# Kernel tuning notes

Measured on AMD Instinct MI355X. Metric: run time of the kernel, lower is better.

## Reference

```python
import jax, jax.numpy as jnp
import numpy as np

D = 1024
H = 16
HD = D // H  # 64


def setup_inputs() -> dict:
    key = jax.random.key(0)
    k1, k2, k3 = jax.random.split(key, 3)
    x = jax.random.normal(k1, (2, 2048, D), dtype=jnp.float32)
    # fused QKV projection weight [d, 3d] and output projection [d, d], no bias
    Wqkv = jax.random.normal(k2, (D, 3 * D), dtype=jnp.float32) * (1.0 / np.sqrt(D))
    Wo = jax.random.normal(k3, (D, D), dtype=jnp.float32) * (1.0 / np.sqrt(D))
    return {"x": x, "Wqkv": Wqkv, "Wo": Wo}


def reference(x, Wqkv, Wo):
    b, t, d = x.shape
    qkv = x @ Wqkv  # [b, t, 3d]
    q, k, v = jnp.split(qkv, 3, axis=-1)
    # [b, t, d] -> [b, h, t, hd]
    def heads(z):
        return z.reshape(b, t, H, HD).transpose(0, 2, 1, 3)
    q, k, v = heads(q), heads(k), heads(v)
    scale = 1.0 / np.sqrt(HD)
    att = jnp.einsum('bhqd,bhkd->bhqk', q, k) * scale  # [b, h, t, t]
    att = jax.nn.softmax(att, axis=-1)
    y = jnp.einsum('bhqk,bhkd->bhqd', att, v)  # [b, h, t, hd]
    y = y.transpose(0, 2, 1, 3).reshape(b, t, d)  # [b, t, d]
    return y @ Wo
```

## Files before the change

### kernel.cpp

```cpp
#include <hip/hip_runtime.h>
#include <hip/hip_bf16.h>

#define D_MODEL 1024
#define NHEADS  16
#define HD      64
#define BATCH   2
#define SEQ     2048
#define NTOK    (BATCH * SEQ)

typedef __attribute__((ext_vector_type(8))) short bf16x8;
typedef __attribute__((ext_vector_type(4))) float f32x4;

#if __has_builtin(__builtin_amdgcn_exp2f)
#define EXP2F(x) __builtin_amdgcn_exp2f(x)
#else
#define EXP2F(x) exp2f(x)
#endif

static __device__ __forceinline__ short f2bf(float f) {
    union { float f; unsigned u; } x; x.f = f;
    unsigned r = (x.u + 0x7fffu + ((x.u >> 16) & 1u)) >> 16;
    return (short)r;
}

static __device__ __forceinline__ unsigned pk_bf16(float a, float b) {
    __hip_bfloat162 h2 = __float22bfloat162_rn(make_float2(a, b));
    union { __hip_bfloat162 h; unsigned u; } c; c.h = h2;
    return c.u;
}

static __device__ __forceinline__ void gl_lds16(const short* g, short* l) {
    __builtin_amdgcn_global_load_lds((const __attribute__((address_space(1))) void*)g,
                                     (__attribute__((address_space(3))) void*)l,
                                     16, 0, 0);
}

__global__ __launch_bounds__(256) void prep_kernel(const float* __restrict__ x,
                                                   short* __restrict__ x_bf,
                                                   const float* __restrict__ Wqkv,
                                                   short* __restrict__ WqkvT,
                                                   const float* __restrict__ Wo,
                                                   short* __restrict__ WoT,
                                                   float cexp) {
    int bid = blockIdx.x;
    int tid = threadIdx.x;

    if (bid < 4096) {
        int i = bid * 256 + tid;
        float4 v = ((const float4*)x)[i];
        short4 o;
        o.x = f2bf(v.x); o.y = f2bf(v.y); o.z = f2bf(v.z); o.w = f2bf(v.w);
        ((short4*)x_bf)[i] = o;
        return;
    }

    __shared__ float tile[32][33];
    const float* in; short* out; int R, C, slimit; float sc; int bx, by;
    if (bid < 4096 + 3072) {
        int idx = bid - 4096;
        in = Wqkv; out = WqkvT; R = D_MODEL; C = 3 * D_MODEL;
        slimit = D_MODEL; sc = cexp;
        bx = idx % 96; by = idx / 96;
    } else {
        int idx = bid - 7168;
        in = Wo; out = WoT; R = D_MODEL; C = D_MODEL;
        slimit = 0; sc = 1.0f;
        bx = idx % 32; by = idx / 32;
    }
    int bc = bx * 32, br = by * 32;
    int tx = tid & 31, ty = tid >> 5;
    #pragma unroll
    for (int i = 0; i < 32; i += 8)
        tile[ty + i][tx] = in[(long)(br + ty + i) * C + bc + tx];
    __syncthreads();
    #pragma unroll
    for (int i = 0; i < 32; i += 8) {
        int orow = bc + ty + i;
        float v = tile[tx][ty + i];
        if (orow < slimit) v *= sc;
        out[(long)orow * R + br + tx] = f2bf(v);
    }
}

__global__ __launch_bounds__(256) void gemm_out(const short* __restrict__ A,
                                                const short* __restrict__ BT,
                                                float* __restrict__ C,
                                                int M, int N, int K) {
    __shared__ short As[128 * 32];
    __shared__ short Bs[64 * 32];

    int tid  = threadIdx.x;
    int lane = tid & 63;
    int w    = tid >> 6;
    int quad = lane >> 4;
    int l16  = lane & 15;

    int m_blk = blockIdx.y * 128, n_blk = blockIdx.x * 64;

    const short* Ag = A  + (long)(m_blk + w * 32 + (lane >> 2)) * K + (lane & 3) * 8;
    const short* Bg = BT + (long)(n_blk + w * 16 + (lane >> 2)) * K + (lane & 3) * 8;
    short* AsW = &As[(w * 32) * 32];
    short* BsW = &Bs[(w * 16) * 32];

    f32x4 acc[2][4] = {};

    for (int k0 = 0; k0 < K; k0 += 32) {
        __syncthreads();
        gl_lds16(Ag + k0,          AsW);
        gl_lds16(Ag + 16 * K + k0, AsW + 16 * 32);
        gl_lds16(Bg + k0,          BsW);
        __syncthreads();

        bf16x8 a[2], b[4];
        #pragma unroll
        for (int i = 0; i < 2; i++)
            a[i] = *(const bf16x8*)&As[(w * 32 + i * 16 + l16) * 32 + quad * 8];
        #pragma unroll
        for (int j = 0; j < 4; j++)
            b[j] = *(const bf16x8*)&Bs[(j * 16 + l16) * 32 + quad * 8];
        #pragma unroll
        for (int i = 0; i < 2; i++)
            #pragma unroll
            for (int j = 0; j < 4; j++)
                acc[i][j] = __builtin_amdgcn_mfma_f32_16x16x32_bf16(a[i], b[j], acc[i][j], 0, 0, 0);
    }

    #pragma unroll
    for (int i = 0; i < 2; i++)
        #pragma unroll
        for (int j = 0; j < 4; j++)
            #pragma unroll
            for (int r = 0; r < 4; r++) {
                int row = m_blk + w * 32 + i * 16 + quad * 4 + r;
                int col = n_blk + j * 16 + l16;
                C[(long)row * N + col] = acc[i][j][r];
            }
}

__global__ __launch_bounds__(256) void gemm_qkv(const short* __restrict__ A,
                                                const short* __restrict__ BT,
                                                short* __restrict__ Qb,
                                                short* __restrict__ Kt2,
                                                short* __restrict__ Vt2) {
    const int K = 1024;
    __shared__ union {
        struct { short As[128 * 32]; short Bs[128 * 32]; } g;
        short Tl[4][64][72];
    } sh;

    int tid  = threadIdx.x;
    int lane = tid & 63;
    int w    = tid >> 6;
    int quad = lane >> 4;
    int l16  = lane & 15;

    int m_blk = blockIdx.y * 128, n_blk = blockIdx.x * 128;
    int mh = (w >> 1) * 64, nh = (w & 1) * 64;

    int sel = blockIdx.x >> 3;
    int ncol0 = n_blk - sel * 1024;

    const short* Ag = A  + (long)(m_blk + w * 32 + (lane >> 2)) * K + (lane & 3) * 8;
    const short* Bg = BT + (long)(n_blk + w * 32 + (lane >> 2)) * K + (lane & 3) * 8;
    short* AsW = &sh.g.As[(w * 32) * 32];
    short* BsW = &sh.g.Bs[(w * 32) * 32];

    f32x4 acc[4][4] = {};

    for (int k0 = 0; k0 < K; k0 += 32) {
        __syncthreads();
        gl_lds16(Ag + k0,          AsW);
        gl_lds16(Ag + 16 * K + k0, AsW + 16 * 32);
        gl_lds16(Bg + k0,          BsW);
        gl_lds16(Bg + 16 * K + k0, BsW + 16 * 32);
        __syncthreads();

        bf16x8 a[4], b[4];
        #pragma unroll
        for (int i = 0; i < 4; i++)
            a[i] = *(const bf16x8*)&sh.g.As[(mh + i * 16 + l16) * 32 + quad * 8];
        #pragma unroll
        for (int j = 0; j < 4; j++)
            b[j] = *(const bf16x8*)&sh.g.Bs[(nh + j * 16 + l16) * 32 + quad * 8];
        #pragma unroll
        for (int i = 0; i < 4; i++)
            #pragma unroll
            for (int j = 0; j < 4; j++)
                acc[i][j] = __builtin_amdgcn_mfma_f32_16x16x32_bf16(a[i], b[j], acc[i][j], 0, 0, 0);
    }

    __syncthreads();

    #pragma unroll
    for (int i = 0; i < 4; i++)
        #pragma unroll
        for (int j = 0; j < 4; j++)
            #pragma unroll
            for (int r = 0; r < 4; r++)
                sh.Tl[w][i * 16 + quad * 4 + r][j * 16 + l16] = f2bf(acc[i][j][r]);

    int R0q = m_blk + mh;
    if (sel == 0) {
        long qbase = (long)R0q * 1024 + (ncol0 + nh);
        #pragma unroll
        for (int ch = 0; ch < 8; ch++) {
            int row  = ch * 8 + (lane >> 3);
            int col0 = (lane & 7) * 8;
            *(bf16x8*)(Qb + qbase + (long)row * 1024 + col0) =
                *(const bf16x8*)&sh.Tl[w][row][col0];
        }
    } else {
        int b2 = R0q >> 11;
        int t  = (R0q & 2047) >> 6;
        int h  = (ncol0 + nh) >> 6;
        long obase = (long)(b2 * 16 + h) * (SEQ * 64) + (long)t * 4096;
        short* outT = (sel == 1) ? Kt2 : Vt2;
        if (sel == 1) {
            #pragma unroll
            for (int ch = 0; ch < 8; ch++) {
                int o = lane * 64 + ch * 8;
                int u = o >> 9, qd = (o >> 7) & 3, l = (o >> 3) & 15;
                int row = (u >> 2) * 32 + ((u >> 1) & 1) * 16 + l;
                int col = (u & 1) * 32 + qd * 8;
                *(bf16x8*)(outT + obase + o) = *(const bf16x8*)&sh.Tl[w][row][col];
            }
        } else {
            #pragma unroll
            for (int ch = 0; ch < 8; ch++) {
                int o = lane * 64 + ch * 8;
                int c = o >> 11, j2 = (o >> 9) & 3, qd = (o >> 7) & 3, l = (o >> 3) & 15;
                int hd = j2 * 16 + l;
                bf16x8 ov;
                #pragma unroll
                for (int jj = 0; jj < 8; jj++) {
                    int s = c * 32 + qd * 8 + jj;
                    int key = (s >> 2) + ((s & 3) << 4);
                    ov[jj] = sh.Tl[w][key][hd];
                }
                *(bf16x8*)(outT + obase + o) = ov;
            }
        }
    }
}

__global__ __launch_bounds__(256, 4) void flash_attn(const short* __restrict__ Qb,
                                                     const short* __restrict__ Kt2,
                                                     const short* __restrict__ Vt2,
                                                     short* __restrict__ y) {
    int tid  = threadIdx.x;
    int lane = tid & 63;
    int w    = tid >> 6;
    int quad = lane >> 4;
    int l16  = lane & 15;
    int qsel = w & 1;
    int ksel = w >> 1;

    int bh = blockIdx.y;
    int b  = bh >> 4;
    int h  = bh & 15;
    int qw = blockIdx.x * 64 + qsel * 32;

    __shared__ union {
        short Ps[4][32 * 72];
        float Mg[2][64][41];
    } sh;
    short* PsW = &sh.Ps[w][0];

    const short* Qrow = Qb + ((long)b * SEQ + qw + l16) * 1024 + h * 64;
    bf16x8 aQ[2][2];
    #pragma unroll
    for (int m = 0; m < 2; m++)
        #pragma unroll
        for (int c = 0; c < 2; c++)
            aQ[m][c] = *(const bf16x8*)(Qrow + (long)(m * 16) * 1024 + c * 32 + quad * 8);

    const short* Ktb = Kt2 + (long)bh * (SEQ * 64) + (long)ksel * 16 * 4096;
    const short* Vtb = Vt2 + (long)bh * (SEQ * 64) + (long)ksel * 16 * 4096;

    f32x4 O[2][4] = {};
    f32x4 Lacc[2] = {};
    bf16x8 ones;
    #pragma unroll
    for (int i = 0; i < 8; i++) ones[i] = (short)0x3F80;

    for (int t = 0; t < 16; t++) {
        const short* Kt = Ktb + t * 4096;
        const short* Vt = Vtb + t * 4096;

        bf16x8 kf[8];
        #pragma unroll
        for (int u = 0; u < 8; u++) kf[u] = *(const bf16x8*)(Kt + u * 512 + lane * 8);

        f32x4 z[2][4];
        #pragma unroll
        for (int m = 0; m < 2; m++)
            #pragma unroll
            for (int kc = 0; kc < 4; kc++) {
                f32x4 zz = {};
                zz = __builtin_amdgcn_mfma_f32_16x16x32_bf16(aQ[m][0], kf[2 * kc],     zz, 0, 0, 0);
                z[m][kc] = __builtin_amdgcn_mfma_f32_16x16x32_bf16(aQ[m][1], kf[2 * kc + 1], zz, 0, 0, 0);
            }

        bf16x8 vf[8];
        #pragma unroll
        for (int u = 0; u < 8; u++) vf[u] = *(const bf16x8*)(Vt + u * 512 + lane * 8);

        #pragma unroll
        for (int m = 0; m < 2; m++)
            #pragma unroll
            for (int r = 0; r < 4; r++) {
                unsigned d0 = pk_bf16(EXP2F(z[m][0][r]), EXP2F(z[m][1][r]));
                unsigned d1 = pk_bf16(EXP2F(z[m][2][r]), EXP2F(z[m][3][r]));
                unsigned long long dd = ((unsigned long long)d1 << 32) | d0;
                *(unsigned long long*)((unsigned*)PsW + (m * 16 + quad * 4 + r) * 36 + 2 * l16) = dd;
            }

        #pragma unroll
        for (int c = 0; c < 2; c++) {
            bf16x8 aP0 = *(const bf16x8*)(PsW + (l16) * 72      + c * 32 + quad * 8);
            bf16x8 aP1 = *(const bf16x8*)(PsW + (16 + l16) * 72 + c * 32 + quad * 8);
            Lacc[0] = __builtin_amdgcn_mfma_f32_16x16x32_bf16(aP0, ones, Lacc[0], 0, 0, 0);
            Lacc[1] = __builtin_amdgcn_mfma_f32_16x16x32_bf16(aP1, ones, Lacc[1], 0, 0, 0);
            #pragma unroll
            for (int j = 0; j < 4; j++) {
                O[0][j] = __builtin_amdgcn_mfma_f32_16x16x32_bf16(aP0, vf[c * 4 + j], O[0][j], 0, 0, 0);
                O[1][j] = __builtin_amdgcn_mfma_f32_16x16x32_bf16(aP1, vf[c * 4 + j], O[1][j], 0, 0, 0);
            }
        }
    }

    __syncthreads();
    if (ksel) {
        float* mg = &sh.Mg[qsel][lane][0];
        #pragma unroll
        for (int m = 0; m < 2; m++)
            #pragma unroll
            for (int j = 0; j < 4; j++)
                #pragma unroll
                for (int r = 0; r < 4; r++)
                    mg[m * 16 + j * 4 + r] = O[m][j][r];
        #pragma unroll
        for (int m = 0; m < 2; m++)
            #pragma unroll
            for (int r = 0; r < 4; r++)
                mg[32 + m * 4 + r] = Lacc[m][r];
    }
    __syncthreads();
    if (!ksel) {
        const float* mg = &sh.Mg[qsel][lane][0];
        #pragma unroll
        for (int m = 0; m < 2; m++)
            #pragma unroll
            for (int j = 0; j < 4; j++)
                #pragma unroll
                for (int r = 0; r < 4; r++)
                    O[m][j][r] += mg[m * 16 + j * 4 + r];
        #pragma unroll
        for (int m = 0; m < 2; m++)
            #pragma unroll
            for (int r = 0; r < 4; r++)
                Lacc[m][r] += mg[32 + m * 4 + r];

        #pragma unroll
        for (int m = 0; m < 2; m++) {
            f32x4 rl;
            #pragma unroll
            for (int r = 0; r < 4; r++) rl[r] = 1.0f / Lacc[m][r];
            #pragma unroll
            for (int j = 0; j < 4; j++)
                #pragma unroll
                for (int r = 0; r < 4; r++) {
                    int row = qw + m * 16 + quad * 4 + r;
                    y[((long)b * SEQ + row) * D_MODEL + h * HD + j * 16 + l16] =
                        f2bf(O[m][j][r] * rl[r]);
                }
        }
    }
}

extern "C" void kernel_launch(void* const* d_in, const int* in_sizes, int n_in,
                              void* d_out, int out_size, void* d_ws, size_t ws_size,
                              hipStream_t stream) {
    const float* x    = (const float*)d_in[0];
    const float* Wqkv = (const float*)d_in[1];
    const float* Wo   = (const float*)d_in[2];

    char* ws = (char*)d_ws;
    short* Qb    = (short*)(ws);
    short* Kt2   = (short*)(ws + 25165824);
    short* Vt2   = (short*)(ws + 33554432);
    short* WqkvT = (short*)(ws + 41943040);
    short* WoT   = (short*)(ws + 48234496);
    short* x_bf  = (short*)d_out;
    short* yb    = (short*)(ws + 8388608);

    const float cexp = 0.125f * 1.4426950408889634f;

    prep_kernel<<<8192, 256, 0, stream>>>(x, x_bf, Wqkv, WqkvT, Wo, WoT, cexp);

    gemm_qkv<<<dim3(3 * D_MODEL / 128, NTOK / 128), 256, 0, stream>>>(
        x_bf, WqkvT, Qb, Kt2, Vt2);

    flash_attn<<<dim3(SEQ / 64, BATCH * NHEADS), 256, 0, stream>>>(Qb, Kt2, Vt2, yb);

    gemm_out<<<dim3(D_MODEL / 64, NTOK / 128), 256, 0, stream>>>(
        yb, WoT, (float*)d_out, NTOK, D_MODEL, D_MODEL);
}
```

Measured before the change: 188.1 us.

## Deepen GEMM K-tiles to 64 and remap QKV blocks across XCDs

Both the QKV and output projection GEMMs now stage two 32-wide K slices per iteration, which halves the number of barrier pairs per K loop and doubles the LDS footprint of the A/B tiles. The QKV GEMM also remaps its linear block id so that consecutive blocks on the same XCD share N-column tiles (3 N tiles per XCD), to improve L2 reuse of weight tiles. The remap assumes a 24x32 grid and round-robin XCD dispatch. The larger LDS use may lower occupancy.

```diff
diff --git a/kernel.cpp b/kernel.cpp
--- a/kernel.cpp
+++ b/kernel.cpp
@@ -86,8 +86,8 @@
                                                 const short* __restrict__ BT,
                                                 float* __restrict__ C,
                                                 int M, int N, int K) {
-    __shared__ short As[128 * 32];
-    __shared__ short Bs[64 * 32];
+    __shared__ short As[2][128 * 32];
+    __shared__ short Bs[2][64 * 32];
 
     int tid  = threadIdx.x;
     int lane = tid & 63;
@@ -99,30 +99,38 @@
 
     const short* Ag = A  + (long)(m_blk + w * 32 + (lane >> 2)) * K + (lane & 3) * 8;
     const short* Bg = BT + (long)(n_blk + w * 16 + (lane >> 2)) * K + (lane & 3) * 8;
-    short* AsW = &As[(w * 32) * 32];
-    short* BsW = &Bs[(w * 16) * 32];
+    short* As0 = &As[0][(w * 32) * 32];
+    short* As1 = &As[1][(w * 32) * 32];
+    short* Bs0 = &Bs[0][(w * 16) * 32];
+    short* Bs1 = &Bs[1][(w * 16) * 32];
 
     f32x4 acc[2][4] = {};
 
-    for (int k0 = 0; k0 < K; k0 += 32) {
+    for (int k0 = 0; k0 < K; k0 += 64) {
         __syncthreads();
-        gl_lds16(Ag + k0,          AsW);
-        gl_lds16(Ag + 16 * K + k0, AsW + 16 * 32);
-        gl_lds16(Bg + k0,          BsW);
+        gl_lds16(Ag + k0,               As0);
+        gl_lds16(Ag + 16 * K + k0,      As0 + 16 * 32);
+        gl_lds16(Ag + k0 + 32,          As1);
+        gl_lds16(Ag + 16 * K + k0 + 32, As1 + 16 * 32);
+        gl_lds16(Bg + k0,               Bs0);
+        gl_lds16(Bg + k0 + 32,          Bs1);
         __syncthreads();
 
-        bf16x8 a[2], b[4];
-        #pragma unroll
-        for (int i = 0; i < 2; i++)
-            a[i] = *(const bf16x8*)&As[(w * 32 + i * 16 + l16) * 32 + quad * 8];
-        #pragma unroll
-        for (int j = 0; j < 4; j++)
-            b[j] = *(const bf16x8*)&Bs[(j * 16 + l16) * 32 + quad * 8];
-        #pragma unroll
-        for (int i = 0; i < 2; i++)
+        #pragma unroll
+        for (int kk = 0; kk < 2; kk++) {
+            bf16x8 a[2], b[4];
+            #pragma unroll
+            for (int i = 0; i < 2; i++)
+                a[i] = *(const bf16x8*)&As[kk][(w * 32 + i * 16 + l16) * 32 + quad * 8];
             #pragma unroll
             for (int j = 0; j < 4; j++)
-                acc[i][j] = __builtin_amdgcn_mfma_f32_16x16x32_bf16(a[i], b[j], acc[i][j], 0, 0, 0);
+                b[j] = *(const bf16x8*)&Bs[kk][(j * 16 + l16) * 32 + quad * 8];
+            #pragma unroll
+            for (int i = 0; i < 2; i++)
+                #pragma unroll
+                for (int j = 0; j < 4; j++)
+                    acc[i][j] = __builtin_amdgcn_mfma_f32_16x16x32_bf16(a[i], b[j], acc[i][j], 0, 0, 0);
+        }
     }
 
     #pragma unroll
@@ -144,7 +152,7 @@
                                                 short* __restrict__ Vt2) {
     const int K = 1024;
     __shared__ union {
-        struct { short As[128 * 32]; short Bs[128 * 32]; } g;
+        struct { short As[2][128 * 32]; short Bs[2][128 * 32]; } g;
         short Tl[4][64][72];
     } sh;
 
@@ -154,39 +162,54 @@
     int quad = lane >> 4;
     int l16  = lane & 15;
 
-    int m_blk = blockIdx.y * 128, n_blk = blockIdx.x * 128;
+    int bid = blockIdx.y * 24 + blockIdx.x;
+    int xcd = bid & 7;
+    int pos = bid >> 3;
+    int nb  = xcd * 3 + (pos % 3);
+    int mb  = pos / 3;
+
+    int m_blk = mb * 128, n_blk = nb * 128;
     int mh = (w >> 1) * 64, nh = (w & 1) * 64;
 
-    int sel = blockIdx.x >> 3;
+    int sel = nb >> 3;
     int ncol0 = n_blk - sel * 1024;
 
     const short* Ag = A  + (long)(m_blk + w * 32 + (lane >> 2)) * K + (lane & 3) * 8;
     const short* Bg = BT + (long)(n_blk + w * 32 + (lane >> 2)) * K + (lane & 3) * 8;
-    short* AsW = &sh.g.As[(w * 32) * 32];
-    short* BsW = &sh.g.Bs[(w * 32) * 32];
+    short* As0 = &sh.g.As[0][(w * 32) * 32];
+    short* As1 = &sh.g.As[1][(w * 32) * 32];
+    short* Bs0 = &sh.g.Bs[0][(w * 32) * 32];
+    short* Bs1 = &sh.g.Bs[1][(w * 32) * 32];
 
     f32x4 acc[4][4] = {};
 
-    for (int k0 = 0; k0 < K; k0 += 32) {
+    for (int k0 = 0; k0 < K; k0 += 64) {
         __syncthreads();
-        gl_lds16(Ag + k0,          AsW);
-        gl_lds16(Ag + 16 * K + k0, AsW + 16 * 32);
-        gl_lds16(Bg + k0,          BsW);
-        gl_lds16(Bg + 16 * K + k0, BsW + 16 * 32);
+        gl_lds16(Ag + k0,               As0);
+        gl_lds16(Ag + 16 * K + k0,      As0 + 16 * 32);
+        gl_lds16(Ag + k0 + 32,          As1);
+        gl_lds16(Ag + 16 * K + k0 + 32, As1 + 16 * 32);
+        gl_lds16(Bg + k0,               Bs0);
+        gl_lds16(Bg + 16 * K + k0,      Bs0 + 16 * 32);
+        gl_lds16(Bg + k0 + 32,          Bs1);
+        gl_lds16(Bg + 16 * K + k0 + 32, Bs1 + 16 * 32);
         __syncthreads();
 
-        bf16x8 a[4], b[4];
-        #pragma unroll
-        for (int i = 0; i < 4; i++)
-            a[i] = *(const bf16x8*)&sh.g.As[(mh + i * 16 + l16) * 32 + quad * 8];
-        #pragma unroll
-        for (int j = 0; j < 4; j++)
-            b[j] = *(const bf16x8*)&sh.g.Bs[(nh + j * 16 + l16) * 32 + quad * 8];
-        #pragma unroll
-        for (int i = 0; i < 4; i++)
+        #pragma unroll
+        for (int kk = 0; kk < 2; kk++) {
+            bf16x8 a[4], b[4];
+            #pragma unroll
+            for (int i = 0; i < 4; i++)
+                a[i] = *(const bf16x8*)&sh.g.As[kk][(mh + i * 16 + l16) * 32 + quad * 8];
             #pragma unroll
             for (int j = 0; j < 4; j++)
-                acc[i][j] = __builtin_amdgcn_mfma_f32_16x16x32_bf16(a[i], b[j], acc[i][j], 0, 0, 0);
+                b[j] = *(const bf16x8*)&sh.g.Bs[kk][(nh + j * 16 + l16) * 32 + quad * 8];
+            #pragma unroll
+            for (int i = 0; i < 4; i++)
+                #pragma unroll
+                for (int j = 0; j < 4; j++)
+                    acc[i][j] = __builtin_amdgcn_mfma_f32_16x16x32_bf16(a[i], b[j], acc[i][j], 0, 0, 0);
+        }
     }
 
     __syncthreads();
```

Result: no change. 188.3 us (+0.1%).
